# Optimization experiments

Hardware: AMD Instinct MI355X
Metric: run time of the kernel (lower is better)

## Reference

```python
import jax, jax.numpy as jnp
import numpy as np

R = 32  # voxel resolution
B, CIN, COUT, N = 4, 64, 64, 4096
K = 3


def setup_inputs():
    key = jax.random.key(0)
    ks = jax.random.split(key, 8)
    s = 0.05
    return {
        "features": jax.random.normal(ks[0], (B, CIN, N), jnp.float32),
        "coords": jax.random.normal(ks[1], (B, 3, N), jnp.float32),
        # voxel branch: conv3d + BN x2
        "w1": jax.random.normal(ks[2], (COUT, CIN, K, K, K), jnp.float32) * s,
        "b1": jnp.zeros((COUT,), jnp.float32),
        "g1": jnp.ones((COUT,), jnp.float32),
        "be1": jnp.zeros((COUT,), jnp.float32),
        "w2": jax.random.normal(ks[3], (COUT, COUT, K, K, K), jnp.float32) * s,
        "b2": jnp.zeros((COUT,), jnp.float32),
        "g2": jnp.ones((COUT,), jnp.float32),
        "be2": jnp.zeros((COUT,), jnp.float32),
        # point branch SharedMLP (1x1 conv + BN + ReLU)
        "wp": jax.random.normal(ks[4], (COUT, CIN), jnp.float32) * s,
        "bp": jnp.zeros((COUT,), jnp.float32),
        "gp": jnp.ones((COUT,), jnp.float32),
        "bep": jnp.zeros((COUT,), jnp.float32),
        # fuzzy_proj 1x1 conv
        "wf": jax.random.normal(ks[5], (COUT, CIN), jnp.float32) * s,
        "bf": jnp.zeros((COUT,), jnp.float32),
        # fusion SharedMLP (3*COUT -> COUT)
        "wfu": jax.random.normal(ks[6], (COUT, 3 * COUT), jnp.float32) * s,
        "bfu": jnp.zeros((COUT,), jnp.float32),
        "gfu": jnp.ones((COUT,), jnp.float32),
        "befu": jnp.zeros((COUT,), jnp.float32),
    }


def _bn3d(x, g, b):
    # training-mode BatchNorm3d, eps=1e-4 (biased variance, as torch)
    m = x.mean((0, 2, 3, 4), keepdims=True)
    v = x.var((0, 2, 3, 4), keepdims=True)
    return (x - m) * jax.lax.rsqrt(v + 1e-4) * g[None, :, None, None, None] + b[None, :, None, None, None]


def _bn1d(x, g, b):
    m = x.mean((0, 2), keepdims=True)
    v = x.var((0, 2), keepdims=True)
    return (x - m) * jax.lax.rsqrt(v + 1e-4) * g[None, :, None] + b[None, :, None]


def _conv3d(x, w, b):
    pad = K // 2
    y = jax.lax.conv_general_dilated(x, w, (1, 1, 1), [(pad, pad)] * 3,
                                     dimension_numbers=('NCDHW', 'OIDHW', 'NCDHW'))
    return y + b[None, :, None, None, None]


def _conv1x1(x, w, b):
    return jnp.einsum('oc,bcn->bon', w, x) + b[None, :, None]


def _voxelize(features, coords):
    # PVCNN Voxelization(normalize=True, eps=0): center, scale to unit, grid coords in [0, R-1]
    nc = coords - coords.mean(axis=2, keepdims=True)              # [B,3,N]
    norm = jnp.linalg.norm(nc, axis=1, keepdims=True)             # [B,1,N]
    nc = nc / (norm.max(axis=2, keepdims=True) * 2.0) + 0.5
    nc = jnp.clip(nc * R, 0.0, R - 1)
    vox = jnp.round(nc).astype(jnp.int32)                         # [B,3,N]
    b_, c_, n_ = features.shape
    idx = (vox[:, 0] * R + vox[:, 1]) * R + vox[:, 2]             # [B,N]
    flat = (idx + jnp.arange(b_)[:, None] * R ** 3).reshape(-1)
    feat = features.transpose(0, 2, 1).reshape(b_ * n_, c_)
    sums = jax.ops.segment_sum(feat, flat, num_segments=b_ * R ** 3)
    cnt = jax.ops.segment_sum(jnp.ones((b_ * n_,), feat.dtype), flat, num_segments=b_ * R ** 3)
    avg = sums / jnp.maximum(cnt, 1.0)[:, None]                   # scatter-mean
    grid = avg.reshape(b_, R ** 3, c_).transpose(0, 2, 1).reshape(b_, c_, R, R, R)
    return grid, nc


def _devoxelize(grid, nc):
    # trilinear gather: grid [B,C,R,R,R], nc [B,3,N] float coords in [0,R-1]
    b_, c_ = grid.shape[:2]
    g = grid.reshape(b_, c_, -1)
    lo_f = jnp.floor(nc)
    fr = nc - lo_f                                                # fractional part [B,3,N]
    lo = lo_f.astype(jnp.int32)
    hi = jnp.minimum(lo + 1, R - 1)
    out = jnp.zeros((b_, c_, nc.shape[2]), grid.dtype)
    for dx in (0, 1):
        for dy in (0, 1):
            for dz in (0, 1):
                ix = hi[:, 0] if dx else lo[:, 0]
                iy = hi[:, 1] if dy else lo[:, 1]
                iz = hi[:, 2] if dz else lo[:, 2]
                w = ((fr[:, 0] if dx else 1.0 - fr[:, 0]) *
                     (fr[:, 1] if dy else 1.0 - fr[:, 1]) *
                     (fr[:, 2] if dz else 1.0 - fr[:, 2]))        # [B,N]
                flat = (ix * R + iy) * R + iz                     # [B,N]
                vals = jnp.take_along_axis(g, flat[:, None, :], axis=2)  # [B,C,N]
                out = out + vals * w[:, None, :]
    return out


def reference(features, coords, w1, b1, g1, be1, w2, b2, g2, be2,
              wp, bp, gp, bep, wf, bf, wfu, bfu, gfu, befu):
    lrelu = lambda x: jnp.where(x > 0, x, 0.1 * x)
    # voxel branch
    grid, nc = _voxelize(features, coords)
    v = lrelu(_bn3d(_conv3d(grid, w1, b1), g1, be1))
    v = lrelu(_bn3d(_conv3d(v, w2, b2), g2, be2))
    vox_feat = _devoxelize(v, nc)                                 # [B,COUT,N]
    # point branch
    pt = jax.nn.relu(_bn1d(_conv1x1(features, wp, bp), gp, bep))
    # fuzzy branch: dense attention over points
    cn = coords.transpose(0, 2, 1)                                # [B,N,3]
    cn = cn / jnp.maximum(jnp.linalg.norm(cn, axis=-1, keepdims=True), 1e-12)
    att = jax.nn.softmax(jnp.einsum('bnd,bmd->bnm', cn, cn) / 0.1, axis=-1)
    fz = jnp.einsum('bnm,bcm->bcn', att, features)                # [B,CIN,N]
    fz = _conv1x1(fz, wf, bf)
    # fusion
    comb = jnp.concatenate([vox_feat, pt, fz], axis=1)            # [B,3*COUT,N]
    fused = jax.nn.relu(_bn1d(_conv1x1(comb, wfu, bfu), gfu, befu))
    return (fused, coords)
```

## Files before the change

kernel.cpp:

```cpp
#include <hip/hip_runtime.h>
#include <hip/hip_bf16.h>
#include <math.h>

#define RR 32
#define R3 32768
#define BB 4
#define CI 64
#define CO 64
#define NN 4096

typedef short v8s __attribute__((ext_vector_type(8)));
typedef float v4f __attribute__((ext_vector_type(4)));
typedef unsigned short ushort_t;

__device__ __forceinline__ unsigned short f2bf(float f) {
    unsigned int u = __float_as_uint(f);
    unsigned int r = (u + 0x7FFFu + ((u >> 16) & 1u)) >> 16;
    return (unsigned short)r;
}
__device__ __forceinline__ float bf2f(unsigned short h) {
    return __uint_as_float((unsigned int)h << 16);
}

__device__ __forceinline__ void gll16(const void* g, void* l) {
    __builtin_amdgcn_global_load_lds((const __attribute__((address_space(1))) unsigned int*)g,
                                     (__attribute__((address_space(3))) unsigned int*)l, 16, 0, 0);
}

__device__ __forceinline__ float blockReduceSum(float v, float* sm) {
    int tid = threadIdx.x;
    sm[tid] = v; __syncthreads();
    for (int off = 128; off > 0; off >>= 1) {
        if (tid < off) sm[tid] += sm[tid + off];
        __syncthreads();
    }
    float r = sm[0]; __syncthreads();
    return r;
}
__device__ __forceinline__ float blockReduceMax(float v, float* sm) {
    int tid = threadIdx.x;
    sm[tid] = v; __syncthreads();
    for (int off = 128; off > 0; off >>= 1) {
        if (tid < off) sm[tid] = fmaxf(sm[tid], sm[tid + off]);
        __syncthreads();
    }
    float r = sm[0]; __syncthreads();
    return r;
}

__global__ void k_nc(const float* __restrict__ coords, float* __restrict__ nc,
                     int* __restrict__ vidx, int* __restrict__ cntI) {
    int b = blockIdx.x, tid = threadIdx.x;
    __shared__ float sm[256];
    const float* cb = coords + (size_t)b * 3 * NN;
    float s0 = 0, s1 = 0, s2 = 0;
    for (int n = tid; n < NN; n += 256) {
        s0 += cb[n]; s1 += cb[NN + n]; s2 += cb[2 * NN + n];
    }
    float m0 = blockReduceSum(s0, sm) * (1.0f / NN);
    float m1 = blockReduceSum(s1, sm) * (1.0f / NN);
    float m2 = blockReduceSum(s2, sm) * (1.0f / NN);
    float mx = 0;
    for (int n = tid; n < NN; n += 256) {
        float dx = cb[n] - m0, dy = cb[NN + n] - m1, dz = cb[2 * NN + n] - m2;
        mx = fmaxf(mx, dx * dx + dy * dy + dz * dz);
    }
    mx = blockReduceMax(mx, sm);
    float denom = 2.0f * sqrtf(mx);
    float mean[3] = {m0, m1, m2};
    for (int n = tid; n < NN; n += 256) {
        int vi[3];
        #pragma unroll
        for (int ax = 0; ax < 3; ax++) {
            float x = (cb[ax * NN + n] - mean[ax]) / denom + 0.5f;
            x = x * RR;
            x = fminf(fmaxf(x, 0.0f), (float)(RR - 1));
            nc[((size_t)b * 3 + ax) * NN + n] = x;
            vi[ax] = (int)rintf(x);
        }
        int idx = (vi[0] * RR + vi[1]) * RR + vi[2];
        vidx[b * NN + n] = idx;
        atomicAdd(&cntI[b * R3 + idx], 1);
    }
}

__global__ void k_scan1(const int* __restrict__ cntI, int* __restrict__ lscan,
                        int* __restrict__ bsum) {
    __shared__ int sm[256];
    int tid = threadIdx.x;
    int i = blockIdx.x * 256 + tid;
    int v = cntI[i];
    sm[tid] = v; __syncthreads();
    for (int off = 1; off < 256; off <<= 1) {
        int t = (tid >= off) ? sm[tid - off] : 0;
        __syncthreads();
        sm[tid] += t;
        __syncthreads();
    }
    lscan[i] = sm[tid] - v;
    if (tid == 255) bsum[blockIdx.x] = sm[tid];
}

__global__ void k_scan2(const int* __restrict__ bsum, int* __restrict__ bbase) {
    __shared__ int sm[512];
    int tid = threadIdx.x;
    int v = bsum[tid];
    sm[tid] = v; __syncthreads();
    for (int off = 1; off < 512; off <<= 1) {
        int t = (tid >= off) ? sm[tid - off] : 0;
        __syncthreads();
        sm[tid] += t;
        __syncthreads();
    }
    bbase[tid] = sm[tid] - v;
}

__global__ void k_fill(const int* __restrict__ vidx, const int* __restrict__ lscan,
                       const int* __restrict__ bbase, int* __restrict__ rank,
                       int* __restrict__ plist) {
    int i = blockIdx.x * 256 + threadIdx.x;
    int b = i >> 12, n = i & (NN - 1);
    int flat = b * R3 + vidx[i];
    int r = atomicAdd(&rank[flat], 1);
    plist[bbase[flat >> 8] + lscan[flat] + r] = n;
}

__global__ void k_pfeat(const float* __restrict__ feat, float* __restrict__ featT,
                        ushort_t* __restrict__ featb) {
    __shared__ float t[64][65];
    int b = blockIdx.y, n0 = blockIdx.x * 64, tid = threadIdx.x;
    int q = tid >> 6, nl = tid & 63;
    #pragma unroll
    for (int k = 0; k < 16; k++) {
        int c = q * 16 + k;
        float v = feat[((size_t)(b * CI + c)) * NN + n0 + nl];
        t[nl][c] = v;
        featb[((size_t)(b * CI + c)) * NN + n0 + nl] = f2bf(v);
    }
    __syncthreads();
    #pragma unroll
    for (int k = 0; k < 16; k++) {
        int n = q * 16 + k;
        featT[((size_t)b * NN + n0 + n) * 64 + nl] = t[n][nl];
    }
}

__global__ __launch_bounds__(256) void k_gather(const float* __restrict__ featT,
                                                const int* __restrict__ cntI,
                                                const int* __restrict__ lscan,
                                                const int* __restrict__ bbase,
                                                const int* __restrict__ plist,
                                                ushort_t* __restrict__ gT) {
    int wv = threadIdx.x >> 6, lane = threadIdx.x & 63;
    int vbase = blockIdx.x * 32 + wv * 8;
    for (int k = 0; k < 8; k++) {
        int flat = vbase + k;
        int count = cntI[flat];
        float s = 0.0f;
        if (count > 0) {
            int b = flat >> 15;
            int start = bbase[flat >> 8] + lscan[flat];
            for (int j = 0; j < count; j++) {
                int n = plist[start + j];
                s += featT[((size_t)b * NN + n) * 64 + lane];
            }
            s *= 1.0f / (float)count;
        }
        gT[(size_t)flat * 64 + lane] = f2bf(s);
    }
}

__global__ void k_tws(const float* __restrict__ w1, const float* __restrict__ w2,
                      ushort_t* __restrict__ wS1, ushort_t* __restrict__ wS2) {
    int i = blockIdx.x * 256 + threadIdx.x;
    const float* w = (i < 110592) ? w1 : w2;
    ushort_t* wS = (i < 110592) ? wS1 : wS2;
    int j = (i < 110592) ? i : i - 110592;
    int cis = j & 31, co = (j >> 5) & 63;
    int dx = (j >> 11) % 3, cih = (j / 6144) & 1, dzdy = j / 12288;
    int k = dzdy * 3 + dx, ci = cih * 32 + cis;
    wS[j] = f2bf(w[((size_t)co * CI + ci) * 27 + k]);
}

__global__ void k_fold(const float* __restrict__ wp, const float* __restrict__ wfu,
                       const float* __restrict__ wf, const float* __restrict__ bf,
                       const float* __restrict__ bfu,
                       float* __restrict__ wpT, float* __restrict__ wfuT,
                       float* __restrict__ bC, float* __restrict__ accs) {
    int i = blockIdx.x * 256 + threadIdx.x;
    if (i < 4096) {
        int c = i >> 6, o = i & 63;
        wpT[c * 64 + o] = wp[o * 64 + c];
    } else if (i < 12288) {
        int j = i - 4096;
        int c = j >> 6, o = j & 63;
        wfuT[c * 64 + o] = wfu[(size_t)o * 192 + c];
    } else if (i < 16384) {
        int j = i - 12288;
        int c = j >> 6, o = j & 63;
        float s = 0;
        for (int k = 0; k < 64; k++)
            s += wfu[(size_t)o * 192 + 128 + k] * wf[(size_t)k * 64 + c];
        wfuT[(128 + c) * 64 + o] = s;
    } else if (i < 16448) {
        int o = i - 16384;
        float s = bfu[o];
        for (int k = 0; k < 64; k++)
            s += wfu[(size_t)o * 192 + 128 + k] * bf[k];
        bC[o] = s;
    } else if (i < 16960) {
        accs[i - 16448] = 0.0f;
    }
}

__global__ void k_bncast2(const ushort_t* __restrict__ x, const float* __restrict__ accs,
                          const float* __restrict__ g, const float* __restrict__ be,
                          float invcnt, float slope, ushort_t* __restrict__ o) {
    size_t i = (size_t)blockIdx.x * 256 + threadIdx.x;
    int c0 = (int)((i * 8) & 63);
    float sc[8], sh[8];
    #pragma unroll
    for (int j = 0; j < 8; j++) {
        int c = c0 + j;
        float mean = accs[2 * c] * invcnt;
        float var = accs[2 * c + 1] * invcnt - mean * mean;
        float scale = g[c] * rsqrtf(var + 1e-4f);
        sc[j] = scale;
        sh[j] = be[c] - mean * scale;
    }
    uint4 in = ((const uint4*)x)[i];
    unsigned iv[4] = {in.x, in.y, in.z, in.w};
    unsigned pk[4];
    #pragma unroll
    for (int j = 0; j < 4; j++) {
        float u0 = bf2f((unsigned short)(iv[j] & 0xFFFF)) * sc[2 * j] + sh[2 * j];
        float u1 = bf2f((unsigned short)(iv[j] >> 16)) * sc[2 * j + 1] + sh[2 * j + 1];
        u0 = u0 > 0 ? u0 : slope * u0;
        u1 = u1 > 0 ? u1 : slope * u1;
        pk[j] = (unsigned)f2bf(u0) | ((unsigned)f2bf(u1) << 16);
    }
    ((uint4*)o)[i] = make_uint4(pk[0], pk[1], pk[2], pk[3]);
}

template <int OUTBF16>
__global__ __launch_bounds__(256) void k_convlds(const ushort_t* __restrict__ gT,
                                                 const ushort_t* __restrict__ wS,
                                                 void* __restrict__ outP,
                                                 float* __restrict__ accs) {
    __shared__ ushort_t lin[20480];
    __shared__ ushort_t lw[2][6144];
    int bid = blockIdx.x;
    int wgid = (bid & 7) * 64 + (bid >> 3);
    int yt = wgid & 3, z0 = (wgid >> 2) & 31, b = wgid >> 7;
    int tid = threadIdx.x;
    int w = __builtin_amdgcn_readfirstlane(tid >> 6);
    int lane = tid & 63, l15 = lane & 15, l4 = lane >> 4;
    int y0 = yt * 8;
    const ushort_t* gTb = gT + (size_t)b * R3 * 64;

    int voxF[4];
    #pragma unroll
    for (int f = 0; f < 4; f++)
        voxF[f] = (w * 2 + (f >> 1)) * 32 + (f & 1) * 16 + l15 - 1;
    bool xlo_ok = (l15 != 0), xhi_ok = (l15 != 15);

    int lsw = lane ^ ((lane >> 3) & 7);
    int wsz8 = ((l15 * 4 + l4) ^ ((l15 >> 1) & 7)) * 8;

    const v8s vzero = {};
    v4f acc[4][4];
    #pragma unroll
    for (int m = 0; m < 4; m++)
        #pragma unroll
        for (int f = 0; f < 4; f++)
            acc[m][f] = (v4f){0.0f, 0.0f, 0.0f, 0.0f};

#define WSTAGE(s)                                                              \
    do {                                                                       \
        const ushort_t* _src = wS + (size_t)(s) * 6144;                        \
        ushort_t* _dst = lw[(s) & 1];                                          \
        _Pragma("unroll") for (int _i = 0; _i < 3; _i++) {                     \
            int _pb = _i * 256 + w * 64;                                       \
            gll16(_src + (size_t)(_pb + lsw) * 8, _dst + (size_t)(_pb + lane) * 8); \
        }                                                                      \
    } while (0)

#define ISTAGE(dz)                                                             \
    do {                                                                       \
        int _zp = z0 - 1 + (dz);                                               \
        if (_zp < 0 || _zp > 31) {                                             \
            for (int _q = 0; _q < 10; _q++)                                    \
                *(v8s*)&lin[(size_t)(w * 640 + _q * 64 + lane) * 8] = vzero;   \
        } else {                                                               \
            if (yt == 0) *(v8s*)&lin[(size_t)tid * 8] = vzero;                 \
            if (yt == 3) *(v8s*)&lin[(size_t)(2304 + tid) * 8] = vzero;        \
            const ushort_t* _pb = gTb + ((size_t)_zp * 1024 + (size_t)(y0 - 1) * 32) * 64; \
            int _g0 = (yt == 0) ? 256 : 0;                                     \
            int _nc = 10 - (yt == 0) - (yt == 3);                              \
            for (int _i = 0; _i < _nc; _i++) {                                 \
                int _pbase = _g0 + _i * 256 + w * 64;                          \
                int _p = _pbase + lane;                                        \
                int _vx = _p >> 3, _js = _p & 7;                               \
                int _sg = _vx * 8 + (_js ^ (_vx & 7));                         \
                gll16(_pb + (size_t)_sg * 8, lin + (size_t)_pbase * 8);        \
            }                                                                  \
        }                                                                      \
    } while (0)

    WSTAGE(0);
    for (int s = 0; s < 18; s++) {
        int dy = (s / 2) % 3, cih = s & 1;
        asm volatile("s_barrier" ::: "memory");
        if ((s % 6) == 0) ISTAGE(s / 6);
        if (s + 1 < 18) WSTAGE(s + 1);
        if (s + 1 < 18) asm volatile("s_waitcnt vmcnt(3) lgkmcnt(0)" ::: "memory");
        else            asm volatile("s_waitcnt vmcnt(0) lgkmcnt(0)" ::: "memory");
        asm volatile("s_barrier" ::: "memory");

        const ushort_t* lwb = lw[s & 1];
        #pragma unroll
        for (int dx = 0; dx < 3; dx++) {
            v8s Bf[4];
            #pragma unroll
            for (int f = 0; f < 4; f++) {
                int vox = voxF[f] + dy * 32 + dx;
                int g = vox * 8 + ((cih * 4 + l4) ^ (vox & 7));
                int bix = g * 16;
                bix = bix < 0 ? 0 : bix;
                v8s vb = *(const v8s*)((const char*)lin + bix);
                bool ok = (dx == 0 && (f & 1) == 0) ? xlo_ok :
                          (dx == 2 && (f & 1) == 1) ? xhi_ok : true;
                Bf[f] = ok ? vb : vzero;
            }
            const ushort_t* ap = lwb + dx * 2048 + wsz8;
            #pragma unroll
            for (int m = 0; m < 4; m++) {
                v8s Af = *(const v8s*)(ap + m * 512);
                #pragma unroll
                for (int f = 0; f < 4; f++)
                    acc[m][f] = __builtin_amdgcn_mfma_f32_16x16x32_bf16(Af, Bf[f], acc[m][f], 0, 0, 0);
            }
        }
    }

    #pragma unroll
    for (int m = 0; m < 4; m++) {
        #pragma unroll
        for (int f = 0; f < 4; f++) {
            int y = y0 + w * 2 + (f >> 1);
            int x = (f & 1) * 16 + l15;
            size_t base = ((size_t)b * R3 + z0 * 1024 + y * 32 + x) * 64 + m * 16 + l4 * 4;
            if (OUTBF16) {
                unsigned p0 = (unsigned)f2bf(acc[m][f][0]) | ((unsigned)f2bf(acc[m][f][1]) << 16);
                unsigned p1 = (unsigned)f2bf(acc[m][f][2]) | ((unsigned)f2bf(acc[m][f][3]) << 16);
                *(uint2*)&((ushort_t*)outP)[base] = make_uint2(p0, p1);
            } else {
                float4 o = make_float4(acc[m][f][0], acc[m][f][1], acc[m][f][2], acc[m][f][3]);
                *(float4*)&((float*)outP)[base] = o;
            }
        }
    }

    __syncthreads();
    float* sbuf = (float*)lin;
    #pragma unroll
    for (int m = 0; m < 4; m++)
        #pragma unroll
        for (int r = 0; r < 4; r++) {
            float s = 0, q = 0;
            #pragma unroll
            for (int f = 0; f < 4; f++) {
                float v = acc[m][f][r];
                s += v; q += v * v;
            }
            sbuf[tid * 32 + (m * 4 + r) * 2] = s;
            sbuf[tid * 32 + (m * 4 + r) * 2 + 1] = q;
        }
    __syncthreads();
    if (tid < 128) {
        int co = tid >> 1, val = tid & 1;
        int m = co >> 4, cl4 = (co >> 2) & 3, r = co & 3;
        float a = 0;
        for (int w2 = 0; w2 < 4; w2++)
            for (int l = 0; l < 16; l++)
                a += sbuf[(w2 * 64 + cl4 * 16 + l) * 32 + (m * 4 + r) * 2 + val];
        atomicAdd(&accs[2 * co + val], a);
    }
#undef WSTAGE
#undef ISTAGE
}

__global__ void k_bnfin2(const float* __restrict__ pst, const float* __restrict__ g,
                         const float* __restrict__ be, float* __restrict__ stats,
                         float invcnt) {
    int c = blockIdx.x, tid = threadIdx.x;
    __shared__ float rs[256], rq[256];
    rs[tid] = pst[(c * 256 + tid) * 2];
    rq[tid] = pst[(c * 256 + tid) * 2 + 1];
    __syncthreads();
    for (int off = 128; off > 0; off >>= 1) {
        if (tid < off) { rs[tid] += rs[tid + off]; rq[tid] += rq[tid + off]; }
        __syncthreads();
    }
    if (tid == 0) {
        float mean = rs[0] * invcnt;
        float var = rq[0] * invcnt - mean * mean;
        float sc = g[c] * rsqrtf(var + 1e-4f);
        stats[2 * c] = sc;
        stats[2 * c + 1] = be[c] - mean * sc;
    }
}

__global__ void k_bn_act(const float* __restrict__ x, const float* __restrict__ stats,
                         float* __restrict__ out, int shift, float slope) {
    size_t i = (size_t)blockIdx.x * 256 + threadIdx.x;
    int c = (int)((i >> shift) & 63);
    float sc = stats[2 * c], sh = stats[2 * c + 1];
    float4 v = ((const float4*)x)[i];
    v.x = v.x * sc + sh; v.y = v.y * sc + sh; v.z = v.z * sc + sh; v.w = v.w * sc + sh;
    v.x = v.x > 0 ? v.x : slope * v.x;
    v.y = v.y > 0 ? v.y : slope * v.y;
    v.z = v.z > 0 ? v.z : slope * v.z;
    v.w = v.w > 0 ? v.w : slope * v.w;
    ((float4*)out)[i] = v;
}

__global__ void k_devox2(const float* __restrict__ gcl, const float* __restrict__ accs,
                         const float* __restrict__ g, const float* __restrict__ be,
                         float invcnt, const float* __restrict__ nc,
                         float* __restrict__ out) {
    int b = blockIdx.y;
    int tid = threadIdx.x, p = tid >> 4, q = tid & 15;
    int n = blockIdx.x * 16 + p;
    float x = nc[((size_t)b * 3 + 0) * NN + n];
    float y = nc[((size_t)b * 3 + 1) * NN + n];
    float z = nc[((size_t)b * 3 + 2) * NN + n];
    float fx = floorf(x), fy = floorf(y), fz = floorf(z);
    int lx = (int)fx, ly = (int)fy, lz = (int)fz;
    int hx = min(lx + 1, RR - 1), hy = min(ly + 1, RR - 1), hz = min(lz + 1, RR - 1);
    float frx = x - fx, fry = y - fy, frz = z - fz;
    int xx[2] = {lx, hx}, yy[2] = {ly, hy}, zz[2] = {lz, hz};
    float wx[2] = {1.0f - frx, frx}, wy[2] = {1.0f - fry, fry}, wz[2] = {1.0f - frz, frz};
    float sc[4], sh[4];
    #pragma unroll
    for (int j = 0; j < 4; j++) {
        int c = q * 4 + j;
        float mean = accs[2 * c] * invcnt;
        float var = accs[2 * c + 1] * invcnt - mean * mean;
        float scale = g[c] * rsqrtf(var + 1e-4f);
        sc[j] = scale;
        sh[j] = be[c] - mean * scale;
    }
    float a0 = 0, a1 = 0, a2 = 0, a3 = 0;
    #pragma unroll
    for (int dx = 0; dx < 2; dx++)
        #pragma unroll
        for (int dy = 0; dy < 2; dy++)
            #pragma unroll
            for (int dz = 0; dz < 2; dz++) {
                int idx = (xx[dx] * RR + yy[dy]) * RR + zz[dz];
                float wt = wx[dx] * wy[dy] * wz[dz];
                float4 v = *(const float4*)&gcl[((size_t)b * R3 + idx) * 64 + q * 4];
                float u0 = v.x * sc[0] + sh[0]; u0 = u0 > 0 ? u0 : 0.1f * u0;
                float u1 = v.y * sc[1] + sh[1]; u1 = u1 > 0 ? u1 : 0.1f * u1;
                float u2 = v.z * sc[2] + sh[2]; u2 = u2 > 0 ? u2 : 0.1f * u2;
                float u3 = v.w * sc[3] + sh[3]; u3 = u3 > 0 ? u3 : 0.1f * u3;
                a0 += wt * u0; a1 += wt * u1; a2 += wt * u2; a3 += wt * u3;
            }
    out[((size_t)(b * 64 + q * 4 + 0)) * NN + n] = a0;
    out[((size_t)(b * 64 + q * 4 + 1)) * NN + n] = a1;
    out[((size_t)(b * 64 + q * 4 + 2)) * NN + n] = a2;
    out[((size_t)(b * 64 + q * 4 + 3)) * NN + n] = a3;
}

__global__ __launch_bounds__(256) void k_fuzzym(const float* __restrict__ coords,
                                                const ushort_t* __restrict__ featb,
                                                float* __restrict__ pnum,
                                                float* __restrict__ pden) {
    __shared__ float cm[3][1024];
    __shared__ ushort_t la[4][2048];
    int b = blockIdx.z, mc = blockIdx.y, nt = blockIdx.x;
    int tid = threadIdx.x;
    int w = tid >> 6, lane = tid & 63, l15 = lane & 15, l4 = lane >> 4;
    int m0 = mc * 1024;

    for (int i = tid; i < 1024; i += 256) {
        float a0 = coords[((size_t)b * 3 + 0) * NN + m0 + i];
        float a1 = coords[((size_t)b * 3 + 1) * NN + m0 + i];
        float a2 = coords[((size_t)b * 3 + 2) * NN + m0 + i];
        float inv = 1.0f / fmaxf(sqrtf(a0 * a0 + a1 * a1 + a2 * a2), 1e-12f);
        cm[0][i] = a0 * inv; cm[1][i] = a1 * inv; cm[2][i] = a2 * inv;
    }

    int n = nt * 64 + w * 16 + l15;
    float q0 = coords[((size_t)b * 3 + 0) * NN + n];
    float q1 = coords[((size_t)b * 3 + 1) * NN + n];
    float q2 = coords[((size_t)b * 3 + 2) * NN + n];
    float qi = 10.0f / fmaxf(sqrtf(q0 * q0 + q1 * q1 + q2 * q2), 1e-12f);
    q0 *= qi; q1 *= qi; q2 *= qi;

    int srow = tid >> 2, sslot = tid & 3;
    int g0 = sslot ^ ((srow >> 1) & 3);
    const ushort_t* fb = featb + (size_t)b * 64 * NN + m0;
    const ushort_t* sbase = fb + (size_t)srow * NN + g0 * 8;
    int rsw = (l15 >> 1) & 3;

    v4f acc[4];
    #pragma unroll
    for (int cb = 0; cb < 4; cb++) acc[cb] = (v4f){0.0f, 0.0f, 0.0f, 0.0f};
    float den = 0.0f;

    gll16(sbase, &la[0][(size_t)tid * 8]);
    gll16(sbase + 32, &la[1][(size_t)tid * 8]);
    gll16(sbase + 64, &la[2][(size_t)tid * 8]);
    __syncthreads();

    for (int t = 0; t < 32; t++) {
        int cur = t & 3;
        asm volatile("s_waitcnt vmcnt(2)" ::: "memory");
        __syncthreads();
        if (t + 3 < 32)
            gll16(sbase + (t + 3) * 32, &la[(t + 3) & 3][(size_t)tid * 8]);

        int mo = t * 32 + l4 * 8;
        float e[8];
        #pragma unroll
        for (int jj = 0; jj < 2; jj++) {
            float4 x0 = *(const float4*)&cm[0][mo + jj * 4];
            float4 x1 = *(const float4*)&cm[1][mo + jj * 4];
            float4 x2 = *(const float4*)&cm[2][mo + jj * 4];
            e[jj * 4 + 0] = __expf(q0 * x0.x + q1 * x1.x + q2 * x2.x);
            e[jj * 4 + 1] = __expf(q0 * x0.y + q1 * x1.y + q2 * x2.y);
            e[jj * 4 + 2] = __expf(q0 * x0.z + q1 * x1.z + q2 * x2.z);
            e[jj * 4 + 3] = __expf(q0 * x0.w + q1 * x1.w + q2 * x2.w);
        }
        den += ((e[0] + e[1]) + (e[2] + e[3])) + ((e[4] + e[5]) + (e[6] + e[7]));
        union { __hip_bfloat162 h[4]; v8s v; } pk;
        pk.h[0] = __float22bfloat162_rn(make_float2(e[0], e[1]));
        pk.h[1] = __float22bfloat162_rn(make_float2(e[2], e[3]));
        pk.h[2] = __float22bfloat162_rn(make_float2(e[4], e[5]));
        pk.h[3] = __float22bfloat162_rn(make_float2(e[6], e[7]));
        #pragma unroll
        for (int cb = 0; cb < 4; cb++) {
            v8s A = *(const v8s*)&la[cur][(size_t)((cb * 16 + l15) * 4 + (l4 ^ rsw)) * 8];
            acc[cb] = __builtin_amdgcn_mfma_f32_16x16x32_bf16(A, pk.v, acc[cb], 0, 0, 0);
        }
        __syncthreads();
    }

    den += __shfl_xor(den, 16);
    den += __shfl_xor(den, 32);

    size_t obase = ((size_t)(b * 4 + mc)) * 64 * NN;
    #pragma unroll
    for (int cb = 0; cb < 4; cb++)
        #pragma unroll
        for (int r = 0; r < 4; r++)
            pnum[obase + (size_t)(cb * 16 + l4 * 4 + r) * NN + n] = acc[cb][r];
    if (l4 == 0) pden[((size_t)(b * 4 + mc)) * NN + n] = den;
}

__global__ void k_combine2(const float* __restrict__ pnum, const float* __restrict__ pden,
                           float* __restrict__ fzf) {
    int i = blockIdx.x * 256 + threadIdx.x;
    int b = i >> 18, c = (i >> 12) & 63, n = i & 4095;
    float num = 0, den = 0;
    #pragma unroll
    for (int ch = 0; ch < 4; ch++) {
        num += pnum[((size_t)(b * 4 + ch) * 64 + c) * NN + n];
        den += pden[((size_t)(b * 4 + ch)) * NN + n];
    }
    fzf[((size_t)(b * 64 + c)) * NN + n] = num / den;
}

__global__ __launch_bounds__(256) void k_1x1s(const float* __restrict__ in,
                                              const float* __restrict__ wT,
                                              const float* __restrict__ bias,
                                              float* __restrict__ out,
                                              float* __restrict__ pst) {
    int b = blockIdx.z, ob = blockIdx.y, bx = blockIdx.x;
    int tid = threadIdx.x;
    int q = tid & 15, o = ob * 16 + (tid >> 4);
    int n = bx * 64 + q * 4;
    const float* src = in + (size_t)b * 64 * NN + n;
    const float* wp_ = wT + o;
    v4f acc = {0, 0, 0, 0};
    #pragma unroll 8
    for (int c = 0; c < 64; c++) {
        float4 x = *(const float4*)&src[(size_t)c * NN];
        float w = wp_[c * 64];
        acc[0] += x.x * w; acc[1] += x.y * w; acc[2] += x.z * w; acc[3] += x.w * w;
    }
    float bv = bias[o];
    float s = 0, q2 = 0;
    float4 ov;
    float* op = (float*)&ov;
    #pragma unroll
    for (int v = 0; v < 4; v++) {
        float val = acc[v] + bv;
        op[v] = val;
        s += val; q2 += val * val;
    }
    *(float4*)&out[((size_t)(b * 64 + o)) * NN + n] = ov;
    #pragma unroll
    for (int off = 1; off < 16; off <<= 1) {
        s += __shfl_xor(s, off);
        q2 += __shfl_xor(q2, off);
    }
    if (q == 0) {
        int part = bx * 4 + b;
        pst[(o * 256 + part) * 2] = s;
        pst[(o * 256 + part) * 2 + 1] = q2;
    }
}

__global__ __launch_bounds__(256) void k_1x1f(const float* __restrict__ vox,
                                              const float* __restrict__ pt,
                                              const float* __restrict__ fzf,
                                              const float* __restrict__ bnB,
                                              const float* __restrict__ wfuT,
                                              const float* __restrict__ bC,
                                              float* __restrict__ out,
                                              float* __restrict__ pst) {
    int b = blockIdx.z, ob = blockIdx.y, bx = blockIdx.x;
    int tid = threadIdx.x;
    int q = tid & 15, o = ob * 16 + (tid >> 4);
    int n = bx * 64 + q * 4;
    const float* srcA = vox + (size_t)b * 64 * NN + n;
    const float* srcB = pt + (size_t)b * 64 * NN + n;
    const float* srcC = fzf + (size_t)b * 64 * NN + n;
    const float* wA = wfuT + o;
    v4f acc = {0, 0, 0, 0};
    #pragma unroll 8
    for (int c = 0; c < 64; c++) {
        float4 x = *(const float4*)&srcA[(size_t)c * NN];
        float w = wA[c * 64];
        acc[0] += x.x * w; acc[1] += x.y * w; acc[2] += x.z * w; acc[3] += x.w * w;
    }
    #pragma unroll 8
    for (int c = 0; c < 64; c++) {
        float4 x = *(const float4*)&srcB[(size_t)c * NN];
        float sc = bnB[2 * c], sh = bnB[2 * c + 1];
        float w = wA[(64 + c) * 64];
        float x0 = fmaxf(x.x * sc + sh, 0.0f), x1 = fmaxf(x.y * sc + sh, 0.0f);
        float x2 = fmaxf(x.z * sc + sh, 0.0f), x3 = fmaxf(x.w * sc + sh, 0.0f);
        acc[0] += x0 * w; acc[1] += x1 * w; acc[2] += x2 * w; acc[3] += x3 * w;
    }
    #pragma unroll 8
    for (int c = 0; c < 64; c++) {
        float4 x = *(const float4*)&srcC[(size_t)c * NN];
        float w = wA[(128 + c) * 64];
        acc[0] += x.x * w; acc[1] += x.y * w; acc[2] += x.z * w; acc[3] += x.w * w;
    }
    float bv = bC[o];
    float s = 0, q2 = 0;
    float4 ov;
    float* op = (float*)&ov;
    #pragma unroll
    for (int v = 0; v < 4; v++) {
        float val = acc[v] + bv;
        op[v] = val;
        s += val; q2 += val * val;
    }
    *(float4*)&out[((size_t)(b * 64 + o)) * NN + n] = ov;
    #pragma unroll
    for (int off = 1; off < 16; off <<= 1) {
        s += __shfl_xor(s, off);
        q2 += __shfl_xor(q2, off);
    }
    if (q == 0) {
        int part = bx * 4 + b;
        pst[(o * 256 + part) * 2] = s;
        pst[(o * 256 + part) * 2 + 1] = q2;
    }
}

extern "C" void kernel_launch(void* const* d_in, const int* in_sizes, int n_in,
                              void* d_out, int out_size, void* d_ws, size_t ws_size,
                              hipStream_t stream) {
    const float* features = (const float*)d_in[0];
    const float* coords = (const float*)d_in[1];
    const float* w1 = (const float*)d_in[2];
    const float* g1 = (const float*)d_in[4];
    const float* be1 = (const float*)d_in[5];
    const float* w2 = (const float*)d_in[6];
    const float* g2 = (const float*)d_in[8];
    const float* be2 = (const float*)d_in[9];
    const float* wp = (const float*)d_in[10];
    const float* bp = (const float*)d_in[11];
    const float* gp = (const float*)d_in[12];
    const float* bep = (const float*)d_in[13];
    const float* wf = (const float*)d_in[14];
    const float* bf = (const float*)d_in[15];
    const float* wfu = (const float*)d_in[16];
    const float* bfu = (const float*)d_in[17];
    const float* gfu = (const float*)d_in[18];
    const float* befu = (const float*)d_in[19];

    float* ws = (float*)d_ws;
    float* nc = ws;
    int* vidx = (int*)(ws + 49152);
    int* cntI = (int*)(ws + 65536);
    float* pden = ws + 65536;
    float* gridCL = ws + 196608;
    ushort_t* gTraw = (ushort_t*)gridCL;
    int* rank = (int*)(ws + 196608);
    int* lscan = (int*)(ws + 327680);
    int* bsum = (int*)(ws + 458752);
    int* bbase = (int*)(ws + 459264);
    int* plist = (int*)(ws + 459776);
    float* featT = ws + 476160;
    float* gTpool = ws + 8585216;
    ushort_t* gT = (ushort_t*)gTpool;
    float* pnum = gTpool;
    float* pstB = gTpool;
    float* stats = ws + 16973824;
    float* voxreg = ws + 16974336;
    ushort_t* wS1 = (ushort_t*)voxreg;
    ushort_t* wS2 = wS1 + 110592;
    float* vox = voxreg;
    float* pt = ws + 18022912;
    float* fzf = ws + 19071488;
    float* wpT = ws + 20120064;
    float* wfuT = wpT + 4096;
    float* bC = wfuT + 12288;
    float* fpre = ws + 21168640;
    ushort_t* featb = (ushort_t*)fpre;
    float* accs = ws + 22217216;

    float* out = (float*)d_out;

    hipMemsetAsync(cntI, 0, (size_t)262144 * 4, stream);

    k_fold<<<67, 256, 0, stream>>>(wp, wfu, wf, bf, bfu, wpT, wfuT, bC, accs);
    k_pfeat<<<dim3(64, BB), 256, 0, stream>>>(features, featT, featb);
    k_tws<<<864, 256, 0, stream>>>(w1, w2, wS1, wS2);

    k_nc<<<BB, 256, 0, stream>>>(coords, nc, vidx, cntI);
    k_scan1<<<512, 256, 0, stream>>>(cntI, lscan, bsum);
    k_scan2<<<1, 512, 0, stream>>>(bsum, bbase);
    k_fill<<<BB * NN / 256, 256, 0, stream>>>(vidx, lscan, bbase, rank, plist);
    k_gather<<<4096, 256, 0, stream>>>(featT, cntI, lscan, bbase, plist, gT);

    k_convlds<1><<<512, 256, 0, stream>>>(gT, wS1, gTraw, accs);
    k_bncast2<<<BB * R3 * 64 / 8 / 256, 256, 0, stream>>>(gTraw, accs, g1, be1,
                                                          1.0f / (BB * R3), 0.1f, gT);
    k_convlds<0><<<512, 256, 0, stream>>>(gT, wS2, gridCL, accs + 128);
    k_devox2<<<dim3(NN / 16, BB), 256, 0, stream>>>(gridCL, accs + 128, g2, be2,
                                                    1.0f / (BB * R3), nc, vox);

    k_fuzzym<<<dim3(64, 4, BB), 256, 0, stream>>>(coords, featb, pnum, pden);
    k_combine2<<<BB * 64 * NN / 256, 256, 0, stream>>>(pnum, pden, fzf);

    k_1x1s<<<dim3(NN / 64, 4, BB), 256, 0, stream>>>(features, wpT, bp, pt, pstB);
    k_bnfin2<<<64, 256, 0, stream>>>(pstB, gp, bep, stats + 256, 1.0f / (BB * NN));

    k_1x1f<<<dim3(NN / 64, 4, BB), 256, 0, stream>>>(vox, pt, fzf, stats + 256, wfuT, bC,
                                                     fpre, pstB);
    k_bnfin2<<<64, 256, 0, stream>>>(pstB, gfu, befu, stats + 384, 1.0f / (BB * NN));
    k_bn_act<<<BB * 64 * NN / 4 / 256, 256, 0, stream>>>(fpre, stats + 384, out, 10, 0.0f);

    hipMemcpyAsync(out + (size_t)BB * CO * NN, coords, (size_t)BB * 3 * NN * 4,
                   hipMemcpyDeviceToDevice, stream);
}
```

Measured before the change: 270.3 us.

## Fuse fuzzy combine into fusion 1x1, store conv2 output as bf16, pad LDS

The separate combine kernel is removed. The fusion 1x1 conv now reads the four per-chunk attention numerators directly and divides by the summed denominators after the projection, which is linear, so the division can be applied at the end. The second 3D conv now writes bf16 output through the raw-cast path, and devoxelize reads bf16. This halves the gather traffic but lowers the precision of the voxel features. The LDS stats buffer stride is padded to 33 to avoid bank conflicts, and workspace offsets and memsets are adjusted. The 1x1f kernel now reads four times more numerator data, which may offset the saved launch and intermediate write.

Result: slower. 327.4 us (+21.1%).

```diff
diff --git a/kernel.cpp b/kernel.cpp
--- a/kernel.cpp
+++ b/kernel.cpp
@@ -373,8 +373,8 @@
                 float v = acc[m][f][r];
                 s += v; q += v * v;
             }
-            sbuf[tid * 32 + (m * 4 + r) * 2] = s;
-            sbuf[tid * 32 + (m * 4 + r) * 2 + 1] = q;
+            sbuf[tid * 33 + (m * 4 + r) * 2] = s;
+            sbuf[tid * 33 + (m * 4 + r) * 2 + 1] = q;
         }
     __syncthreads();
     if (tid < 128) {
@@ -383,7 +383,7 @@
         float a = 0;
         for (int w2 = 0; w2 < 4; w2++)
             for (int l = 0; l < 16; l++)
-                a += sbuf[(w2 * 64 + cl4 * 16 + l) * 32 + (m * 4 + r) * 2 + val];
+                a += sbuf[(w2 * 64 + cl4 * 16 + l) * 33 + (m * 4 + r) * 2 + val];
         atomicAdd(&accs[2 * co + val], a);
     }
 #undef WSTAGE
@@ -425,7 +425,7 @@
     ((float4*)out)[i] = v;
 }
 
-__global__ void k_devox2(const float* __restrict__ gcl, const float* __restrict__ accs,
+__global__ void k_devox2(const ushort_t* __restrict__ gcl, const float* __restrict__ accs,
                          const float* __restrict__ g, const float* __restrict__ be,
                          float invcnt, const float* __restrict__ nc,
                          float* __restrict__ out) {
@@ -460,11 +460,15 @@
             for (int dz = 0; dz < 2; dz++) {
                 int idx = (xx[dx] * RR + yy[dy]) * RR + zz[dz];
                 float wt = wx[dx] * wy[dy] * wz[dz];
-                float4 v = *(const float4*)&gcl[((size_t)b * R3 + idx) * 64 + q * 4];
-                float u0 = v.x * sc[0] + sh[0]; u0 = u0 > 0 ? u0 : 0.1f * u0;
-                float u1 = v.y * sc[1] + sh[1]; u1 = u1 > 0 ? u1 : 0.1f * u1;
-                float u2 = v.z * sc[2] + sh[2]; u2 = u2 > 0 ? u2 : 0.1f * u2;
-                float u3 = v.w * sc[3] + sh[3]; u3 = u3 > 0 ? u3 : 0.1f * u3;
+                uint2 pv = *(const uint2*)&gcl[((size_t)b * R3 + idx) * 64 + q * 4];
+                float v0 = bf2f((unsigned short)(pv.x & 0xFFFF));
+                float v1 = bf2f((unsigned short)(pv.x >> 16));
+                float v2 = bf2f((unsigned short)(pv.y & 0xFFFF));
+                float v3 = bf2f((unsigned short)(pv.y >> 16));
+                float u0 = v0 * sc[0] + sh[0]; u0 = u0 > 0 ? u0 : 0.1f * u0;
+                float u1 = v1 * sc[1] + sh[1]; u1 = u1 > 0 ? u1 : 0.1f * u1;
+                float u2 = v2 * sc[2] + sh[2]; u2 = u2 > 0 ? u2 : 0.1f * u2;
+                float u3 = v3 * sc[3] + sh[3]; u3 = u3 > 0 ? u3 : 0.1f * u3;
                 a0 += wt * u0; a1 += wt * u1; a2 += wt * u2; a3 += wt * u3;
             }
     out[((size_t)(b * 64 + q * 4 + 0)) * NN + n] = a0;
@@ -558,19 +562,6 @@
         for (int r = 0; r < 4; r++)
             pnum[obase + (size_t)(cb * 16 + l4 * 4 + r) * NN + n] = acc[cb][r];
     if (l4 == 0) pden[((size_t)(b * 4 + mc)) * NN + n] = den;
-}
-
-__global__ void k_combine2(const float* __restrict__ pnum, const float* __restrict__ pden,
-                           float* __restrict__ fzf) {
-    int i = blockIdx.x * 256 + threadIdx.x;
-    int b = i >> 18, c = (i >> 12) & 63, n = i & 4095;
-    float num = 0, den = 0;
-    #pragma unroll
-    for (int ch = 0; ch < 4; ch++) {
-        num += pnum[((size_t)(b * 4 + ch) * 64 + c) * NN + n];
-        den += pden[((size_t)(b * 4 + ch)) * NN + n];
-    }
-    fzf[((size_t)(b * 64 + c)) * NN + n] = num / den;
 }
 
 __global__ __launch_bounds__(256) void k_1x1s(const float* __restrict__ in,
@@ -616,7 +607,8 @@
 
 __global__ __launch_bounds__(256) void k_1x1f(const float* __restrict__ vox,
                                               const float* __restrict__ pt,
-                                              const float* __restrict__ fzf,
+                                              const float* __restrict__ pnum,
+                                              const float* __restrict__ pden,
                                               const float* __restrict__ bnB,
                                               const float* __restrict__ wfuT,
                                               const float* __restrict__ bC,
@@ -628,7 +620,6 @@
     int n = bx * 64 + q * 4;
     const float* srcA = vox + (size_t)b * 64 * NN + n;
     const float* srcB = pt + (size_t)b * 64 * NN + n;
-    const float* srcC = fzf + (size_t)b * 64 * NN + n;
     const float* wA = wfuT + o;
     v4f acc = {0, 0, 0, 0};
     #pragma unroll 8
@@ -646,12 +637,25 @@
         float x2 = fmaxf(x.z * sc + sh, 0.0f), x3 = fmaxf(x.w * sc + sh, 0.0f);
         acc[0] += x0 * w; acc[1] += x1 * w; acc[2] += x2 * w; acc[3] += x3 * w;
     }
-    #pragma unroll 8
-    for (int c = 0; c < 64; c++) {
-        float4 x = *(const float4*)&srcC[(size_t)c * NN];
-        float w = wA[(128 + c) * 64];
-        acc[0] += x.x * w; acc[1] += x.y * w; acc[2] += x.z * w; acc[3] += x.w * w;
-    }
+    v4f accC = {0, 0, 0, 0};
+    float4 den4 = make_float4(0, 0, 0, 0);
+    #pragma unroll
+    for (int ch = 0; ch < 4; ch++) {
+        float4 d = *(const float4*)&pden[((size_t)(b * 4 + ch)) * NN + n];
+        den4.x += d.x; den4.y += d.y; den4.z += d.z; den4.w += d.w;
+        const float* srcC = pnum + ((size_t)(b * 4 + ch) * 64) * NN + n;
+        #pragma unroll 8
+        for (int c = 0; c < 64; c++) {
+            float4 x = *(const float4*)&srcC[(size_t)c * NN];
+            float w = wA[(128 + c) * 64];
+            accC[0] += x.x * w; accC[1] += x.y * w; accC[2] += x.z * w; accC[3] += x.w * w;
+        }
+    }
+    acc[0] += accC[0] / den4.x;
+    acc[1] += accC[1] / den4.y;
+    acc[2] += accC[2] / den4.z;
+    acc[3] += accC[3] / den4.w;
+
     float bv = bC[o];
     float s = 0, q2 = 0;
     float4 ov;
@@ -713,26 +717,24 @@
     float* gTpool = ws + 8585216;
     ushort_t* gT = (ushort_t*)gTpool;
     float* pnum = gTpool;
-    float* pstB = gTpool;
+    float* pstB = gTpool + 4194304;
     float* stats = ws + 16973824;
     float* voxreg = ws + 16974336;
     ushort_t* wS1 = (ushort_t*)voxreg;
     ushort_t* wS2 = wS1 + 110592;
     float* vox = voxreg;
     float* pt = ws + 18022912;
-    float* fzf = ws + 19071488;
-    float* wpT = ws + 20120064;
-    float* wfuT = wpT + 4096;
-    float* bC = wfuT + 12288;
     float* fpre = ws + 21168640;
     ushort_t* featb = (ushort_t*)fpre;
     float* accs = ws + 22217216;
 
     float* out = (float*)d_out;
 
-    hipMemsetAsync(cntI, 0, (size_t)262144 * 4, stream);
-
-    k_fold<<<67, 256, 0, stream>>>(wp, wfu, wf, bf, bfu, wpT, wfuT, bC, accs);
+    hipMemsetAsync(cntI, 0, (size_t)131072 * 4, stream);
+    hipMemsetAsync(rank, 0, (size_t)131072 * 4, stream);
+
+    k_fold<<<67, 256, 0, stream>>>(wp, wfu, wf, bf, bfu,
+                                   ws + 20120064, ws + 20124160, ws + 20136448, accs);
     k_pfeat<<<dim3(64, BB), 256, 0, stream>>>(features, featT, featb);
     k_tws<<<864, 256, 0, stream>>>(w1, w2, wS1, wS2);
 
@@ -745,17 +747,17 @@
     k_convlds<1><<<512, 256, 0, stream>>>(gT, wS1, gTraw, accs);
     k_bncast2<<<BB * R3 * 64 / 8 / 256, 256, 0, stream>>>(gTraw, accs, g1, be1,
                                                           1.0f / (BB * R3), 0.1f, gT);
-    k_convlds<0><<<512, 256, 0, stream>>>(gT, wS2, gridCL, accs + 128);
-    k_devox2<<<dim3(NN / 16, BB), 256, 0, stream>>>(gridCL, accs + 128, g2, be2,
+    k_convlds<1><<<512, 256, 0, stream>>>(gT, wS2, gTraw, accs + 128);
+    k_devox2<<<dim3(NN / 16, BB), 256, 0, stream>>>(gTraw, accs + 128, g2, be2,
                                                     1.0f / (BB * R3), nc, vox);
 
     k_fuzzym<<<dim3(64, 4, BB), 256, 0, stream>>>(coords, featb, pnum, pden);
-    k_combine2<<<BB * 64 * NN / 256, 256, 0, stream>>>(pnum, pden, fzf);
-
-    k_1x1s<<<dim3(NN / 64, 4, BB), 256, 0, stream>>>(features, wpT, bp, pt, pstB);
+
+    k_1x1s<<<dim3(NN / 64, 4, BB), 256, 0, stream>>>(features, ws + 20120064, bp, pt, pstB);
     k_bnfin2<<<64, 256, 0, stream>>>(pstB, gp, bep, stats + 256, 1.0f / (BB * NN));
 
-    k_1x1f<<<dim3(NN / 64, 4, BB), 256, 0, stream>>>(vox, pt, fzf, stats + 256, wfuT, bC,
+    k_1x1f<<<dim3(NN / 64, 4, BB), 256, 0, stream>>>(vox, pt, pnum, pden, stats + 256,
+                                                     ws + 20124160, ws + 20136448,
                                                      fpre, pstB);
     k_bnfin2<<<64, 256, 0, stream>>>(pstB, gfu, befu, stats + 384, 1.0f / (BB * NN));
     k_bn_act<<<BB * 64 * NN / 4 / 256, 256, 0, stream>>>(fpre, stats + 384, out, 10, 0.0f);
```
